# Kernel optimization log

Hardware: AMD Instinct MI355X
Metric: run time of the kernel (lower is better)

Reference implementation:

```python
import jax, jax.numpy as jnp
import numpy as np

M = 8
EPS = 1e-5


def _bn(x, gamma, beta):
    # x: [T, N, C]; torch BatchNorm1d on [T, C, N] (training mode) normalizes
    # over batch and length dims -> axes (0, 1) here, biased variance.
    mean = jnp.mean(x, axis=(0, 1))
    var = jnp.var(x, axis=(0, 1))
    return (x - mean) * jax.lax.rsqrt(var + EPS) * gamma + beta


def setup_inputs() -> dict:
    key = jax.random.key(0)
    T, N, E = 128, 256, 128
    ks = jax.random.split(key, 16)
    s = 1.0 / np.sqrt(E)
    inp = {
        "node": jax.random.normal(ks[0], (T, N, E), dtype=jnp.float32),
        "Wq": jax.random.uniform(ks[1], (E, E), jnp.float32, -s, s),
        "bq": jax.random.uniform(ks[2], (E,), jnp.float32, -s, s),
        "Wk": jax.random.uniform(ks[3], (E, E), jnp.float32, -s, s),
        "bk": jax.random.uniform(ks[4], (E,), jnp.float32, -s, s),
        "Wv": jax.random.uniform(ks[5], (E, E), jnp.float32, -s, s),
        "bv": jax.random.uniform(ks[6], (E,), jnp.float32, -s, s),
        "Ww": jax.random.uniform(ks[7], (E, E), jnp.float32, -s, s),
        "bw": jax.random.uniform(ks[8], (E,), jnp.float32, -s, s),
        "Wf1": jax.random.uniform(ks[9], (4 * E, E), jnp.float32, -s, s),
        "bf1": jax.random.uniform(ks[10], (4 * E,), jnp.float32, -s, s),
        "Wf2": jax.random.uniform(ks[11], (E, 4 * E), jnp.float32, -0.5 * s, 0.5 * s),
        "bf2": jax.random.uniform(ks[12], (E,), jnp.float32, -0.5 * s, 0.5 * s),
        "g1": jnp.ones((E,), jnp.float32),
        "be1": jnp.zeros((E,), jnp.float32),
        "g2": jnp.ones((E,), jnp.float32),
        "be2": jnp.zeros((E,), jnp.float32),
        "temp_len": T,
    }
    return inp


def reference(node, Wq, bq, Wk, bk, Wv, bv, Ww, bw, Wf1, bf1, Wf2, bf2,
              g1, be1, g2, be2, temp_len):
    T, N, E = node.shape
    D = E // M          # head dim = 16
    dk = E / M          # softmax scale denominator (embedding_size / M)

    q = (node @ Wq.T + bq).reshape(T, N, M, D)
    k = (node @ Wk.T + bk).reshape(T, N, M, D)
    v = (node @ Wv.T + bv).reshape(T, N, M, D)

    # scores[t,n,j,m] = sum_d q[t,n,m,d]*k[t,j,m,d] / sqrt(dk)
    scores = jnp.einsum('tnmd,tjmd->tnjm', q, k) / jnp.sqrt(jnp.float32(dk))
    attn = jax.nn.softmax(scores, axis=2)  # softmax over key dim (dim=2)

    # out[t,n,m,d] = sum_j attn[t,n,j,m] * v[t,j,m,d]
    out = jnp.einsum('tnjm,tjmd->tnmd', attn, v).reshape(T, N, E)

    x = out @ Ww.T + bw + node
    x = _bn(x, g1, be1)

    x1 = jax.nn.relu(x @ Wf1.T + bf1) @ Wf2.T + bf2
    x = x + x1
    x = _bn(x, g2, be2)
    return x
```

## Files before the change

### kernel.cpp

```cpp
#include <hip/hip_runtime.h>
#include <stdint.h>

typedef unsigned int  uint32;
typedef unsigned short u16;
typedef __attribute__((ext_vector_type(8))) short short8;
typedef __attribute__((ext_vector_type(4))) float f32x4;
typedef __attribute__((ext_vector_type(4))) _Float16 half4;

__device__ __forceinline__ float bits2f(uint32 u){ union{uint32 u; float f;} c; c.u=u; return c.f; }
__device__ __forceinline__ uint32 f2bits(float f){ union{uint32 u; float f;} c; c.f=f; return c.u; }
__device__ __forceinline__ u16 f2b(float f){ uint32 u=f2bits(f); return (u16)((u + 0x7FFFu + ((u>>16)&1u))>>16); }
__device__ __forceinline__ float b2f(u16 h){ return bits2f(((uint32)h)<<16); }
__device__ __forceinline__ u16 f2h(float f){ _Float16 h=(_Float16)f; union{u16 u; _Float16 h;} c; c.h=h; return c.u; }
__device__ __forceinline__ float4 ld4f(const float* p){ return *(const float4*)p; }
#define BLO(u) bits2f((u)<<16)
#define BHI(u) bits2f((u)&0xFFFF0000u)

#define QKS 24

__device__ __forceinline__ void load_ab(const float* __restrict__ gacc,
                                        const float* __restrict__ gam,
                                        const float* __restrict__ bet,
                                        float* sA, float* sB, int t)
{
  if (t < 128) {
    const float mean = gacc[t] * (1.f/32768.f);
    const float var  = gacc[128 + t] * (1.f/32768.f) - mean * mean;
    const float rstd = rsqrtf(var + 1e-5f);
    const float Ac = gam[t] * rstd;
    sA[t] = Ac;
    sB[t] = bet[t] - mean * Ac;
  }
  __syncthreads();
}

template<int OMODE, int RES, bool RELU, bool AF32, bool WF32, bool BNA, bool STATS, int JT>
__device__ __forceinline__ void gemm_tile(
    u16* As, u16* Ws, const float* sA, const float* sB, float* pS, float* pQ,
    const void* Ain, const void* W, const float* bias, const void* res,
    float* gacc_out, void* out, int row0, int col0, int K, int Nout,
    float oscale, int t)
{
  constexpr int WROWS = JT * 32;
  const int L = t & 63, w = t >> 6;
  const int wrow = (w >> 1) * 64, wcol = (w & 1) * (JT * 16);
  const int lm = L & 15, lg = L >> 4;

  f32x4 acc[4][JT];
#pragma unroll
  for (int i = 0; i < 4; ++i)
#pragma unroll
    for (int j = 0; j < JT; ++j) acc[i][j] = (f32x4){0.f,0.f,0.f,0.f};

  const int srow = t >> 1, skc = (t & 1) * 32;
  const u16*   Ab = (const u16*)Ain + (size_t)(row0 + srow) * K + skc;
  const float* Af = (const float*)Ain + (size_t)(row0 + srow) * K + skc;
  u16* Asp = As + srow * 72 + skc;
  constexpr int TPR = 256 / WROWS;
  const int wsrow = t / TPR, wskc = (t % TPR) * (64 / TPR);
  const u16*   Wp  = (const u16*)W + (size_t)(col0 + wsrow) * K + wskc;
  const float* Wpf = (const float*)W + (size_t)(col0 + wsrow) * K + wskc;
  u16* Wsp = Ws + wsrow * 72 + wskc;
  constexpr int NW = (64 / TPR) / 8;

  short8 ga[4]; short8 gw[NW];
  float4 fa[4][2]; float4 fw[NW][2];

  auto load_chunk = [&](int k0) {
    if constexpr (AF32) {
#pragma unroll
      for (int i = 0; i < 4; ++i) {
        fa[i][0] = ld4f(Af + k0 + i*8);
        fa[i][1] = ld4f(Af + k0 + i*8 + 4);
      }
    } else {
#pragma unroll
      for (int i = 0; i < 4; ++i) ga[i] = *(const short8*)(Ab + k0 + i*8);
    }
    if constexpr (WF32) {
#pragma unroll
      for (int i = 0; i < NW; ++i) {
        fw[i][0] = ld4f(Wpf + k0 + i*8);
        fw[i][1] = ld4f(Wpf + k0 + i*8 + 4);
      }
    } else {
#pragma unroll
      for (int i = 0; i < NW; ++i) gw[i] = *(const short8*)(Wp + k0 + i*8);
    }
  };

  auto write_chunk = [&](int k0) {
    if constexpr (AF32) {
#pragma unroll
      for (int i = 0; i < 4; ++i) {
        short8 s;
        s[0]=(short)f2b(fa[i][0].x); s[1]=(short)f2b(fa[i][0].y);
        s[2]=(short)f2b(fa[i][0].z); s[3]=(short)f2b(fa[i][0].w);
        s[4]=(short)f2b(fa[i][1].x); s[5]=(short)f2b(fa[i][1].y);
        s[6]=(short)f2b(fa[i][1].z); s[7]=(short)f2b(fa[i][1].w);
        *(short8*)(Asp + i*8) = s;
      }
    } else if constexpr (BNA) {
#pragma unroll
      for (int i = 0; i < 4; ++i) {
        const int c = skc + k0 + i*8;
        const short8 x8 = ga[i];
        const float4 A0 = *(const float4*)&sA[c], A1 = *(const float4*)&sA[c+4];
        const float4 B0 = *(const float4*)&sB[c], B1 = *(const float4*)&sB[c+4];
        short8 s;
        s[0]=(short)f2b(b2f((u16)x8[0])*A0.x+B0.x); s[1]=(short)f2b(b2f((u16)x8[1])*A0.y+B0.y);
        s[2]=(short)f2b(b2f((u16)x8[2])*A0.z+B0.z); s[3]=(short)f2b(b2f((u16)x8[3])*A0.w+B0.w);
        s[4]=(short)f2b(b2f((u16)x8[4])*A1.x+B1.x); s[5]=(short)f2b(b2f((u16)x8[5])*A1.y+B1.y);
        s[6]=(short)f2b(b2f((u16)x8[6])*A1.z+B1.z); s[7]=(short)f2b(b2f((u16)x8[7])*A1.w+B1.w);
        *(short8*)(Asp + i*8) = s;
      }
    } else {
#pragma unroll
      for (int i = 0; i < 4; ++i) *(short8*)(Asp + i*8) = ga[i];
    }
    if constexpr (WF32) {
#pragma unroll
      for (int i = 0; i < NW; ++i) {
        short8 s;
        s[0]=(short)f2b(fw[i][0].x); s[1]=(short)f2b(fw[i][0].y);
        s[2]=(short)f2b(fw[i][0].z); s[3]=(short)f2b(fw[i][0].w);
        s[4]=(short)f2b(fw[i][1].x); s[5]=(short)f2b(fw[i][1].y);
        s[6]=(short)f2b(fw[i][1].z); s[7]=(short)f2b(fw[i][1].w);
        *(short8*)(Wsp + i*8) = s;
      }
    } else {
#pragma unroll
      for (int i = 0; i < NW; ++i) *(short8*)(Wsp + i*8) = gw[i];
    }
  };

  load_chunk(0);
  for (int k0 = 0; k0 < K; k0 += 64) {
    __syncthreads();
    write_chunk(k0);
    __syncthreads();
    if (k0 + 64 < K) load_chunk(k0 + 64);
#pragma unroll
    for (int ks = 0; ks < 64; ks += 32) {
      short8 af[4], wf[JT];
#pragma unroll
      for (int i = 0; i < 4; ++i)
        af[i] = *(const short8*)(As + (wrow + i*16 + lm) * 72 + ks + lg*8);
#pragma unroll
      for (int j = 0; j < JT; ++j)
        wf[j] = *(const short8*)(Ws + (wcol + j*16 + lm) * 72 + ks + lg*8);
#pragma unroll
      for (int i = 0; i < 4; ++i)
#pragma unroll
        for (int j = 0; j < JT; ++j)
          acc[i][j] = __builtin_amdgcn_mfma_f32_16x16x32_bf16(af[i], wf[j], acc[i][j], 0, 0, 0);
    }
  }

  float bj[JT];
#pragma unroll
  for (int j = 0; j < JT; ++j) bj[j] = bias[col0 + wcol + j*16 + lm];

  float stS[JT], stQ[JT];
#pragma unroll
  for (int j = 0; j < JT; ++j) { stS[j] = 0.f; stQ[j] = 0.f; }

#pragma unroll
  for (int i = 0; i < 4; ++i) {
    const int rowb = row0 + wrow + i*16 + lg*4;
#pragma unroll
    for (int j = 0; j < JT; ++j) {
      const int col = col0 + wcol + j*16 + lm;
      float ra = 0.f, rb = 0.f;
      if constexpr (RES == 3) { ra = sA[col & 127]; rb = sB[col & 127]; }
      if constexpr (OMODE == 3) {
        const int tt = rowb >> 8, n0 = rowb & 255;
        const int mh = col >> 4, d = col & 15;
        uint2 o;
        o.x = (uint32)f2h(acc[i][j][0] + bj[j]) | ((uint32)f2h(acc[i][j][1] + bj[j]) << 16);
        o.y = (uint32)f2h(acc[i][j][2] + bj[j]) | ((uint32)f2h(acc[i][j][3] + bj[j]) << 16);
        *(uint2*)((u16*)out + (((size_t)tt*8 + mh)*16 + d)*256 + n0) = o;
      } else {
#pragma unroll
        for (int r = 0; r < 4; ++r) {
          const int row = rowb + r;
          float v = acc[i][j][r] + bj[j];
          if constexpr (RES == 1) v += ((const float*)res)[(size_t)row*128 + col];
          if constexpr (RES == 3) v += b2f(((const u16*)res)[(size_t)row*128 + col]) * ra + rb;
          if constexpr (RELU) v = fmaxf(v, 0.f);
          if constexpr (STATS) { stS[j] += v; stQ[j] += v*v; }
          if constexpr (OMODE == 2) {
            const int tt = row >> 8, n = row & 255, mh = col >> 4, d = col & 15;
            ((u16*)out)[(((size_t)tt*8 + mh)*256 + n)*16 + d] = f2h(v * oscale);
          } else {
            ((u16*)out)[(size_t)row * Nout + col] = f2b(v);
          }
        }
      }
    }
  }

  if constexpr (STATS) {
    __syncthreads();
    if (t < 128) { pS[t] = 0.f; pQ[t] = 0.f; }
    __syncthreads();
#pragma unroll
    for (int j = 0; j < JT; ++j) {
      const int col = col0 + wcol + j*16 + lm;
      atomicAdd(&pS[col], stS[j]);
      atomicAdd(&pQ[col], stQ[j]);
    }
    __syncthreads();
    if (t < 128) {
      atomicAdd(&gacc_out[t],       pS[t]);
      atomicAdd(&gacc_out[128 + t], pQ[t]);
    }
  }
}

__global__ __launch_bounds__(256)
void qkv_k(const float* __restrict__ node,
           const float* __restrict__ Wq, const float* __restrict__ bq,
           const float* __restrict__ Wk, const float* __restrict__ bk,
           const float* __restrict__ Wv, const float* __restrict__ bv,
           const float* __restrict__ Ww, const float* __restrict__ Wf1,
           const float* __restrict__ Wf2,
           u16* __restrict__ qb, u16* __restrict__ kb, u16* __restrict__ vb,
           u16* __restrict__ wb, float* __restrict__ accbuf)
{
  const int bid = blockIdx.x, t = threadIdx.x;
  if (bid < 768) {
    __shared__ u16 As[128*72];
    __shared__ u16 Ws[128*72];
    __shared__ __align__(16) float sA[128], sB[128];
    __shared__ float pS[128], pQ[128];
    const int x = bid & 255, y = bid >> 8;
    const float QSCALE = 0.36067376022224085f;
    if (y == 0)
      gemm_tile<2,0,false,true,true,false,false,4>(As,Ws,sA,sB,pS,pQ, node, Wq, bq,
          nullptr, nullptr, qb, x*128, 0, 128, 128, QSCALE, t);
    else if (y == 1)
      gemm_tile<2,0,false,true,true,false,false,4>(As,Ws,sA,sB,pS,pQ, node, Wk, bk,
          nullptr, nullptr, kb, x*128, 0, 128, 128, 1.f, t);
    else
      gemm_tile<3,0,false,true,true,false,false,4>(As,Ws,sA,sB,pS,pQ, node, Wv, bv,
          nullptr, nullptr, vb, x*128, 0, 128, 128, 1.f, t);
  } else if (bid < 912) {
    const int i = (bid - 768) * 256 + t;
    const float4* src; u16* dst;
    if      (i <  4096) { src = (const float4*)Ww  + i;         dst = wb +  49152 + (size_t)i*4; }
    else if (i < 20480) { src = (const float4*)Wf1 + (i-4096);  dst = wb +  65536 + (size_t)(i-4096)*4; }
    else                { src = (const float4*)Wf2 + (i-20480); dst = wb + 131072 + (size_t)(i-20480)*4; }
    float4 v = *src;
    uint2 o;
    o.x = (uint32)f2b(v.x) | ((uint32)f2b(v.y) << 16);
    o.y = (uint32)f2b(v.z) | ((uint32)f2b(v.w) << 16);
    *(uint2*)dst = o;
  } else {
    accbuf[t] = 0.f;
    accbuf[256 + t] = 0.f;
  }
}

__global__ __launch_bounds__(256)
void oproj_k(const u16* __restrict__ ab, const u16* __restrict__ wwb,
             const float* __restrict__ bw, const float* __restrict__ node,
             float* __restrict__ accbuf, u16* __restrict__ xb)
{
  __shared__ u16 As[128*72];
  __shared__ u16 Ws[64*72];
  __shared__ __align__(16) float sA[128], sB[128];
  __shared__ float pS[128], pQ[128];
  gemm_tile<0,1,false,false,false,false,true,2>(As,Ws,sA,sB,pS,pQ, ab, wwb, bw,
      node, accbuf, xb, blockIdx.x*128, blockIdx.y*64, 128, 128, 1.f, threadIdx.x);
}

__global__ __launch_bounds__(256)
void ffn1_k(const u16* __restrict__ xb, const u16* __restrict__ wf1b,
            const float* __restrict__ bf1, const float* __restrict__ accbuf,
            const float* __restrict__ g1, const float* __restrict__ be1,
            u16* __restrict__ hb)
{
  __shared__ u16 As[128*72];
  __shared__ u16 Ws[128*72];
  __shared__ __align__(16) float sA[128], sB[128];
  __shared__ float pS[128], pQ[128];
  load_ab(accbuf, g1, be1, sA, sB, threadIdx.x);
  gemm_tile<0,0,true,false,false,true,false,4>(As,Ws,sA,sB,pS,pQ, xb, wf1b, bf1,
      nullptr, nullptr, hb, blockIdx.x*128, blockIdx.y*128, 128, 512, 1.f, threadIdx.x);
}

__global__ __launch_bounds__(256)
void ffn2_k(const u16* __restrict__ hb, const u16* __restrict__ wf2b,
            const float* __restrict__ bf2, const u16* __restrict__ xb,
            const float* __restrict__ accbuf, const float* __restrict__ g1,
            const float* __restrict__ be1, float* __restrict__ acc2,
            u16* __restrict__ x2b)
{
  __shared__ u16 As[128*72];
  __shared__ u16 Ws[64*72];
  __shared__ __align__(16) float sA[128], sB[128];
  __shared__ float pS[128], pQ[128];
  load_ab(accbuf, g1, be1, sA, sB, threadIdx.x);
  gemm_tile<0,3,false,false,false,false,true,2>(As,Ws,sA,sB,pS,pQ, hb, wf2b, bf2,
      xb, acc2, x2b, blockIdx.x*128, blockIdx.y*64, 512, 128, 1.f, threadIdx.x);
}

__global__ __launch_bounds__(256)
void attn_k(const u16* __restrict__ q, const u16* __restrict__ k,
            const u16* __restrict__ v, u16* __restrict__ ab)
{
  __shared__ __align__(16) u16 Qs[256*QKS];
  __shared__ __align__(16) u16 Ks[256*QKS];
  __shared__ __align__(16) u16 Vt[16*264];
  const int tm = blockIdx.x, tt = tm >> 3, m = tm & 7;
  const int t = threadIdx.x;

  const uint4* qg = (const uint4*)(q + (size_t)tm*4096);
  const uint4* kg = (const uint4*)(k + (size_t)tm*4096);
  const uint4* vg = (const uint4*)(v + (size_t)tm*4096);
#pragma unroll
  for (int p = t; p < 512; p += 256) {
    const uint4 a = qg[p], b = kg[p], c = vg[p];
    const int row = p >> 1, h = (p & 1) * 8;
    *(uint4*)(Qs + row*QKS + h) = a;
    *(uint4*)(Ks + row*QKS + h) = b;
    *(uint4*)(Vt + (p >> 5)*264 + (p & 31)*8) = c;
  }
  __syncthreads();

  const int w = t >> 6, L = t & 63, lm = L & 15, quad = L >> 4;

  half4 vf[16];
#pragma unroll
  for (int jt = 0; jt < 16; ++jt)
    vf[jt] = *(const half4*)(Vt + lm*264 + jt*16 + quad*4);

  for (int nt = 0; nt < 4; ++nt) {
    const half4 bq = *(const half4*)(Qs + ((w*4 + nt)*16 + lm)*QKS + quad*4);
    f32x4 s[16];
#pragma unroll
    for (int jt = 0; jt < 16; ++jt) {
      const half4 af = *(const half4*)(Ks + (jt*16 + lm)*QKS + quad*4);
      s[jt] = __builtin_amdgcn_mfma_f32_16x16x16f16(af, bq, (f32x4){0.f,0.f,0.f,0.f}, 0, 0, 0);
    }
    float mx = s[0][0];
#pragma unroll
    for (int jt = 0; jt < 16; ++jt)
#pragma unroll
      for (int r = 0; r < 4; ++r) mx = fmaxf(mx, s[jt][r]);
    mx = fmaxf(mx, __shfl_xor(mx, 16));
    mx = fmaxf(mx, __shfl_xor(mx, 32));
    float ls = 0.f;
#pragma unroll
    for (int jt = 0; jt < 16; ++jt)
#pragma unroll
      for (int r = 0; r < 4; ++r) { const float p = exp2f(s[jt][r] - mx); s[jt][r] = p; ls += p; }
    ls += __shfl_xor(ls, 16);
    ls += __shfl_xor(ls, 32);

    f32x4 oacc = {0.f,0.f,0.f,0.f};
#pragma unroll
    for (int jt = 0; jt < 16; ++jt) {
      half4 pf;
      pf[0] = (_Float16)s[jt][0]; pf[1] = (_Float16)s[jt][1];
      pf[2] = (_Float16)s[jt][2]; pf[3] = (_Float16)s[jt][3];
      oacc = __builtin_amdgcn_mfma_f32_16x16x16f16(pf, vf[jt], oacc, 0, 0, 0);
    }
    const int q0 = w*64 + nt*16 + quad*4;
#pragma unroll
    for (int r = 0; r < 4; ++r) {
      const float lr = __shfl(ls, quad*4 + r);
      ab[((size_t)tt*256 + q0 + r)*128 + m*16 + lm] = f2b(oacc[r] / lr);
    }
  }
}

__global__ __launch_bounds__(256)
void bn_final(const uint2* __restrict__ x2, const float* __restrict__ gacc,
              const float* __restrict__ gam, const float* __restrict__ bet,
              float* __restrict__ out)
{
  __shared__ __align__(16) float sA[128], sB[128];
  const int t = threadIdx.x;
  load_ab(gacc, gam, bet, sA, sB, t);
#pragma unroll 2
  for (int kk = 0; kk < 8; ++kk) {
    const size_t idx = (size_t)blockIdx.x * 2048 + kk * 256 + t;
    const uint2 u = x2[idx];
    const int c = (int)((idx & 31) * 4);
    const f32x4 A = *(const f32x4*)&sA[c];
    const f32x4 B = *(const f32x4*)&sB[c];
    f32x4 o;
    o[0] = BLO(u.x)*A[0] + B[0];
    o[1] = BHI(u.x)*A[1] + B[1];
    o[2] = BLO(u.y)*A[2] + B[2];
    o[3] = BHI(u.y)*A[3] + B[3];
    *(f32x4*)(out + idx*4) = o;
  }
}

extern "C" void kernel_launch(void* const* d_in, const int* in_sizes, int n_in,
                              void* d_out, int out_size, void* d_ws, size_t ws_size,
                              hipStream_t stream)
{
  (void)in_sizes; (void)n_in; (void)out_size; (void)ws_size;
  const float* node = (const float*)d_in[0];
  const float* Wq  = (const float*)d_in[1];  const float* bq  = (const float*)d_in[2];
  const float* Wk  = (const float*)d_in[3];  const float* bk  = (const float*)d_in[4];
  const float* Wv  = (const float*)d_in[5];  const float* bv  = (const float*)d_in[6];
  const float* Ww  = (const float*)d_in[7];  const float* bw  = (const float*)d_in[8];
  const float* Wf1 = (const float*)d_in[9];  const float* bf1 = (const float*)d_in[10];
  const float* Wf2 = (const float*)d_in[11]; const float* bf2 = (const float*)d_in[12];
  const float* g1  = (const float*)d_in[13]; const float* be1 = (const float*)d_in[14];
  const float* g2  = (const float*)d_in[15]; const float* be2 = (const float*)d_in[16];
  float* out = (float*)d_out;
  char* ws = (char*)d_ws;

  u16* wb  = (u16*)(ws + 0);
  u16* qb  = (u16*)(ws + 524288);
  u16* kb  = (u16*)(ws + 8912896);
  u16* vb  = (u16*)(ws + 17301504);
  u16* ab  = (u16*)(ws + 25690112);
  u16* xb  = (u16*)(ws + 34078720);
  u16* x2b = (u16*)(ws + 42467328);
  float* accbuf = (float*)(ws + 50855936);
  u16* hb  = qb;

  u16* wwb = wb + 49152;  u16* wf1b = wb + 65536; u16* wf2b = wb + 131072;

  dim3 blk(256);

  qkv_k<<<dim3(913), blk, 0, stream>>>(node, Wq,bq, Wk,bk, Wv,bv, Ww, Wf1, Wf2,
                                       qb, kb, vb, wb, accbuf);
  attn_k<<<dim3(1024), blk, 0, stream>>>(qb, kb, vb, ab);
  oproj_k<<<dim3(256,2), blk, 0, stream>>>(ab, wwb, bw, node, accbuf, xb);
  ffn1_k<<<dim3(256,4), blk, 0, stream>>>(xb, wf1b, bf1, accbuf, g1, be1, hb);
  ffn2_k<<<dim3(256,2), blk, 0, stream>>>(hb, wf2b, bf2, xb, accbuf, g1, be1,
                                          accbuf + 256, x2b);
  bn_final<<<dim3(512), blk, 0, stream>>>((const uint2*)x2b, accbuf + 256, g2, be2, out);
}
```

Before: 209.5 us.

## Fuse FFN1 and FFN2 into one kernel keeping hidden activations in LDS

Replaces the two FFN GEMM kernels with a single 512-thread kernel per 64-row tile. The BN1-normalized input is staged in shared memory, the ReLU hidden layer (64x512 bf16) is written to LDS instead of global memory, and then consumed directly by the second GEMM along with the residual and BN2 statistics. This removes the global round trip of the 32 MB hidden tensor and one launch. In exchange it uses a large LDS footprint (about 100 KB), which limits occupancy, and weights stream through a single-buffered tile with syncs every chunk.

```diff
diff --git a/kernel.cpp b/kernel.cpp
--- a/kernel.cpp
+++ b/kernel.cpp
@@ -275,35 +275,124 @@
       node, accbuf, xb, blockIdx.x*128, blockIdx.y*64, 128, 128, 1.f, threadIdx.x);
 }
 
-__global__ __launch_bounds__(256)
-void ffn1_k(const u16* __restrict__ xb, const u16* __restrict__ wf1b,
-            const float* __restrict__ bf1, const float* __restrict__ accbuf,
-            const float* __restrict__ g1, const float* __restrict__ be1,
-            u16* __restrict__ hb)
-{
-  __shared__ u16 As[128*72];
-  __shared__ u16 Ws[128*72];
+#define HS_LD 520
+#define AS_LD 136
+#define WS_LD 72
+
+__global__ __launch_bounds__(512)
+void ffn_k(const u16* __restrict__ xb, const u16* __restrict__ wf1b,
+           const float* __restrict__ bf1, const u16* __restrict__ wf2b,
+           const float* __restrict__ bf2, const float* __restrict__ accbuf,
+           const float* __restrict__ g1, const float* __restrict__ be1,
+           float* __restrict__ acc2, u16* __restrict__ x2b)
+{
+  __shared__ u16 Hs[64*HS_LD];
+  __shared__ u16 As[64*AS_LD];
+  __shared__ u16 Ws[128*WS_LD];
   __shared__ __align__(16) float sA[128], sB[128];
   __shared__ float pS[128], pQ[128];
-  load_ab(accbuf, g1, be1, sA, sB, threadIdx.x);
-  gemm_tile<0,0,true,false,false,true,false,4>(As,Ws,sA,sB,pS,pQ, xb, wf1b, bf1,
-      nullptr, nullptr, hb, blockIdx.x*128, blockIdx.y*128, 128, 512, 1.f, threadIdx.x);
-}
-
-__global__ __launch_bounds__(256)
-void ffn2_k(const u16* __restrict__ hb, const u16* __restrict__ wf2b,
-            const float* __restrict__ bf2, const u16* __restrict__ xb,
-            const float* __restrict__ accbuf, const float* __restrict__ g1,
-            const float* __restrict__ be1, float* __restrict__ acc2,
-            u16* __restrict__ x2b)
-{
-  __shared__ u16 As[128*72];
-  __shared__ u16 Ws[64*72];
-  __shared__ __align__(16) float sA[128], sB[128];
-  __shared__ float pS[128], pQ[128];
-  load_ab(accbuf, g1, be1, sA, sB, threadIdx.x);
-  gemm_tile<0,3,false,false,false,false,true,2>(As,Ws,sA,sB,pS,pQ, hb, wf2b, bf2,
-      xb, acc2, x2b, blockIdx.x*128, blockIdx.y*64, 512, 128, 1.f, threadIdx.x);
+
+  const int t = threadIdx.x;
+  const int row0 = blockIdx.x * 64;
+  load_ab(accbuf, g1, be1, sA, sB, t);
+
+  {
+    const int r = t >> 3, seg = (t & 7) * 16;
+    const u16* src = xb + (size_t)(row0 + r) * 128 + seg;
+    u16* dst = As + r * AS_LD + seg;
+#pragma unroll
+    for (int h = 0; h < 2; ++h) {
+      const short8 x8 = *(const short8*)(src + h*8);
+      const int c = seg + h*8;
+      const float4 A0 = *(const float4*)&sA[c], A1 = *(const float4*)&sA[c+4];
+      const float4 B0 = *(const float4*)&sB[c], B1 = *(const float4*)&sB[c+4];
+      short8 s;
+      s[0]=(short)f2b(b2f((u16)x8[0])*A0.x+B0.x); s[1]=(short)f2b(b2f((u16)x8[1])*A0.y+B0.y);
+      s[2]=(short)f2b(b2f((u16)x8[2])*A0.z+B0.z); s[3]=(short)f2b(b2f((u16)x8[3])*A0.w+B0.w);
+      s[4]=(short)f2b(b2f((u16)x8[4])*A1.x+B1.x); s[5]=(short)f2b(b2f((u16)x8[5])*A1.y+B1.y);
+      s[6]=(short)f2b(b2f((u16)x8[6])*A1.z+B1.z); s[7]=(short)f2b(b2f((u16)x8[7])*A1.w+B1.w);
+      *(short8*)(dst + h*8) = s;
+    }
+  }
+
+  const int w = t >> 6, L = t & 63, lm = L & 15, lg = L >> 4;
+  const int wcol = w * 16;
+  const int wr = t >> 2, kc = (t & 3) * 16;
+
+  auto wsrc = [&](int cc) -> const u16* {
+    if (cc < 8) return wf1b + (size_t)((cc>>1)*128 + wr)*128 + (cc&1)*64 + kc;
+    return wf2b + (size_t)wr*512 + (cc-8)*64 + kc;
+  };
+
+  f32x4 accF[4];
+#pragma unroll
+  for (int i = 0; i < 4; ++i) accF[i] = (f32x4){0.f,0.f,0.f,0.f};
+
+  short8 gw0 = *(const short8*)(wsrc(0));
+  short8 gw1 = *(const short8*)(wsrc(0) + 8);
+
+  for (int cc = 0; cc < 16; ++cc) {
+    __syncthreads();
+    *(short8*)(Ws + wr*WS_LD + kc)     = gw0;
+    *(short8*)(Ws + wr*WS_LD + kc + 8) = gw1;
+    __syncthreads();
+    if (cc < 15) {
+      gw0 = *(const short8*)(wsrc(cc+1));
+      gw1 = *(const short8*)(wsrc(cc+1) + 8);
+    }
+    const u16* Abase = (cc < 8) ? (As + ((size_t)(cc & 1) * 64))
+                                : (Hs + ((size_t)(cc - 8) * 64));
+    const int ald = (cc < 8) ? AS_LD : HS_LD;
+#pragma unroll
+    for (int ks = 0; ks < 64; ks += 32) {
+      short8 af[4], wf;
+#pragma unroll
+      for (int i = 0; i < 4; ++i)
+        af[i] = *(const short8*)(Abase + (i*16 + lm) * ald + ks + lg*8);
+      wf = *(const short8*)(Ws + (wcol + lm) * WS_LD + ks + lg*8);
+#pragma unroll
+      for (int i = 0; i < 4; ++i)
+        accF[i] = __builtin_amdgcn_mfma_f32_16x16x32_bf16(af[i], wf, accF[i], 0, 0, 0);
+    }
+    if (cc < 8 && (cc & 1)) {
+      const int ct = cc >> 1;
+      const float b1 = bf1[ct*128 + wcol + lm];
+#pragma unroll
+      for (int i = 0; i < 4; ++i) {
+#pragma unroll
+        for (int r = 0; r < 4; ++r) {
+          const int row = i*16 + lg*4 + r;
+          Hs[row*HS_LD + ct*128 + wcol + lm] = f2b(fmaxf(accF[i][r] + b1, 0.f));
+        }
+        accF[i] = (f32x4){0.f,0.f,0.f,0.f};
+      }
+    }
+  }
+
+  const int col = wcol + lm;
+  const float b2 = bf2[col];
+  const float ra = sA[col], rb = sB[col];
+  float stS = 0.f, stQ = 0.f;
+#pragma unroll
+  for (int i = 0; i < 4; ++i) {
+#pragma unroll
+    for (int r = 0; r < 4; ++r) {
+      const int row = row0 + i*16 + lg*4 + r;
+      float v = accF[i][r] + b2 + b2f(xb[(size_t)row*128 + col]) * ra + rb;
+      stS += v; stQ += v*v;
+      x2b[(size_t)row*128 + col] = f2b(v);
+    }
+  }
+  __syncthreads();
+  if (t < 128) { pS[t] = 0.f; pQ[t] = 0.f; }
+  __syncthreads();
+  atomicAdd(&pS[col], stS);
+  atomicAdd(&pQ[col], stQ);
+  __syncthreads();
+  if (t < 128) {
+    atomicAdd(&acc2[t],       pS[t]);
+    atomicAdd(&acc2[128 + t], pQ[t]);
+  }
 }
 
 __global__ __launch_bounds__(256)
@@ -425,7 +514,6 @@
   u16* xb  = (u16*)(ws + 34078720);
   u16* x2b = (u16*)(ws + 42467328);
   float* accbuf = (float*)(ws + 50855936);
-  u16* hb  = qb;
 
   u16* wwb = wb + 49152;  u16* wf1b = wb + 65536; u16* wf2b = wb + 131072;
 
@@ -435,8 +523,7 @@
                                        qb, kb, vb, wb, accbuf);
   attn_k<<<dim3(1024), blk, 0, stream>>>(qb, kb, vb, ab);
   oproj_k<<<dim3(256,2), blk, 0, stream>>>(ab, wwb, bw, node, accbuf, xb);
-  ffn1_k<<<dim3(256,4), blk, 0, stream>>>(xb, wf1b, bf1, accbuf, g1, be1, hb);
-  ffn2_k<<<dim3(256,2), blk, 0, stream>>>(hb, wf2b, bf2, xb, accbuf, g1, be1,
-                                          accbuf + 256, x2b);
+  ffn_k<<<dim3(512), dim3(512), 0, stream>>>(xb, wf1b, bf1, wf2b, bf2,
+                                             accbuf, g1, be1, accbuf + 256, x2b);
   bn_final<<<dim3(512), blk, 0, stream>>>((const uint2*)x2b, accbuf + 256, g2, be2, out);
 }
```

New measurement: 210.7 us. About the same (+0.6%).
